# Performance work log

Measured on AMD Instinct MI355X. Metric: run time of the kernel, lower is better.

## Reference

```python
import jax, jax.numpy as jnp
import numpy as np

N_EMBD = 512
N_EXPERTS = 4
TOP_K = 2
D_FF = 4 * N_EMBD


def setup_inputs() -> dict:
    key = jax.random.key(0)
    k_x, k_g, k_w1, k_w2 = jax.random.split(key, 4)
    b, t = 8, 2048
    x = jax.random.normal(k_x, (b, t, N_EMBD), dtype=jnp.float32)
    # Linear layers are bias-free; kaiming-uniform-ish init scale
    gate_w = jax.random.normal(k_g, (N_EMBD, N_EXPERTS), dtype=jnp.float32) * (1.0 / np.sqrt(N_EMBD))
    w1 = jax.random.normal(k_w1, (N_EXPERTS, N_EMBD, D_FF), dtype=jnp.float32) * (1.0 / np.sqrt(N_EMBD))
    w2 = jax.random.normal(k_w2, (N_EXPERTS, D_FF, N_EMBD), dtype=jnp.float32) * (1.0 / np.sqrt(D_FF))
    return {"x": x, "gate_w": gate_w, "w1": w1, "w2": w2}


def reference(x, gate_w, w1, w2):
    # Eval mode: UnitCenteredNoise and Dropout are identity.
    b, t, c = x.shape
    xf = x.reshape(b * t, c)                         # [N, C]
    n = xf.shape[0]

    gate_logits = xf @ gate_w                        # [N, E]
    gate_probs = jax.nn.softmax(gate_logits, axis=-1)
    top_w, top_i = jax.lax.top_k(gate_probs, TOP_K)  # [N, K]
    top_w = top_w / jnp.clip(jnp.sum(top_w, axis=-1, keepdims=True), 1e-6)

    # Sparse router weights [N, E]: zeros except normalized top-k probs.
    router_sparse = jnp.zeros((n, N_EXPERTS), dtype=top_w.dtype)
    router_sparse = router_sparse.at[jnp.arange(n)[:, None], top_i].set(top_w)

    # Per-expert MLP on all tokens, combined with the sparse router weights.
    # Mathematically identical to the masked dispatch/combine in the original.
    h = jnp.einsum('nc,ech->enh', xf, w1)            # [E, N, 4C]
    h = jax.nn.gelu(h, approximate=False)            # torch F.gelu default = erf
    y = jnp.einsum('enh,ehc->enc', h, w2)            # [E, N, C]
    out_flat = jnp.einsum('ne,enc->nc', router_sparse, y)

    return out_flat.reshape(b, t, c), router_sparse
```

## Files before the change

### kernel.cpp

```cpp
#include <hip/hip_runtime.h>
#include <hip/hip_fp16.h>


#define NTOK  16384
#define CDIM  512
#define FF    2048
#define NEXP  4
#define CAP   33280
#define NBLK  260
#define BM    128
#define BN1   128
#define BN2   128
#define BK    32
#define CPAD  32

typedef _Float16 f16;
typedef __attribute__((ext_vector_type(8))) _Float16 f16x8;
typedef __attribute__((ext_vector_type(4))) _Float16 f16x4;
typedef __attribute__((ext_vector_type(4))) float f32x4;

__device__ __forceinline__ void gload16(const void* g, void* l) {
  __builtin_amdgcn_global_load_lds(
      (const __attribute__((address_space(1))) unsigned int*)g,
      (__attribute__((address_space(3))) unsigned int*)l, 16, 0, 0);
}

__device__ __forceinline__ float gelu_fast(float v) {
  float az = fabsf(v) * 0.7071067811865476f;
  float t = __builtin_amdgcn_rcpf(fmaf(0.3275911f, az, 1.0f));
  float p = fmaf(fmaf(fmaf(fmaf(1.061405429f, t, -1.453152027f), t,
                           1.421413741f), t, -0.284496736f), t, 0.254829592f) * t;
  float e = __builtin_amdgcn_exp2f(az * az * -1.4426950408889634f);
  float erfa = fmaf(-p, e, 1.0f);
  float u = copysignf(erfa, v);
  return 0.5f * v * (1.0f + u);
}

__device__ __forceinline__ int xcd_swz(int bid, int nwg) {
  int q = nwg >> 3, r = nwg & 7;
  int x = bid & 7, o = bid >> 3;
  return (x < r ? x * (q + 1) : r * (q + 1) + (x - r) * q) + o;
}


__global__ __launch_bounds__(256) void k_init(int* list, int* cnt) {
  int i = blockIdx.x * 256 + threadIdx.x;
  if (i < CAP) list[i] = -1;
  if (i < 4) cnt[i * CPAD] = 0;
}

__global__ __launch_bounds__(256) void k_cast_t(const float* __restrict__ in,
                                                f16* __restrict__ out, int R, int Cc) {
  __shared__ f16 T[64][72];
  int ez = blockIdx.z;
  const float* ine = in + (size_t)ez * R * Cc;
  f16* oute = out + (size_t)ez * R * Cc;
  int c0 = blockIdx.x * 64;
  int r0 = blockIdx.y * 64;
  int t = threadIdx.x;
  {
    int rr = t >> 2, cc = (t & 3) * 16;
    const float* src = ine + (size_t)(r0 + rr) * Cc + c0 + cc;
    union { f16 h[16]; uint4 u[2]; } pk;
#pragma unroll
    for (int j = 0; j < 16; j += 4) {
      float4 a = *(const float4*)(src + j);
      pk.h[j] = (f16)a.x; pk.h[j + 1] = (f16)a.y;
      pk.h[j + 2] = (f16)a.z; pk.h[j + 3] = (f16)a.w;
    }
    *(uint4*)&T[rr][cc] = pk.u[0];
    *(uint4*)&T[rr][cc + 8] = pk.u[1];
  }
  __syncthreads();
  {
    int oc = t >> 2, orr = (t & 3) * 16;
    union { f16 h[16]; uint4 u[2]; } pk;
#pragma unroll
    for (int j = 0; j < 16; ++j) pk.h[j] = T[orr + j][oc];
    f16* dst = oute + (size_t)(c0 + oc) * R + r0 + orr;
    *(uint4*)dst = pk.u[0];
    *(uint4*)(dst + 8) = pk.u[1];
  }
}


__global__ __launch_bounds__(256) void k_router(const float* __restrict__ x,
                                                const float* __restrict__ gw,
                                                f16* __restrict__ xh,
                                                float* __restrict__ rout,
                                                float4* __restrict__ tokinfo,
                                                int* __restrict__ cnt) {
  __shared__ int lcnt[4];
  int tid = threadIdx.x;
  if (tid < 4) lcnt[tid] = 0;
  __syncthreads();
  int wv = tid >> 6, lane = tid & 63;
  const float4* g = ((const float4*)gw) + lane * 8;
  float4 gv[8];
#pragma unroll
  for (int j = 0; j < 8; ++j) gv[j] = g[j];

  int tok0 = blockIdx.x * 64 + wv * 16;
  for (int i = 0; i < 16; ++i) {
    int tok = tok0 + i;
    const float4* xr = (const float4*)(x + (size_t)tok * CDIM + lane * 8);
    float4 a0 = xr[0], a1 = xr[1];
    union { f16 h[8]; uint4 u; } pk;
    pk.h[0] = (f16)a0.x; pk.h[1] = (f16)a0.y; pk.h[2] = (f16)a0.z; pk.h[3] = (f16)a0.w;
    pk.h[4] = (f16)a1.x; pk.h[5] = (f16)a1.y; pk.h[6] = (f16)a1.z; pk.h[7] = (f16)a1.w;
    *(uint4*)(xh + (size_t)tok * CDIM + lane * 8) = pk.u;
    float xv[8] = {a0.x, a0.y, a0.z, a0.w, a1.x, a1.y, a1.z, a1.w};
    float l0 = 0, l1 = 0, l2 = 0, l3 = 0;
#pragma unroll
    for (int j = 0; j < 8; ++j) {
      float4 g4 = gv[j];
      l0 = fmaf(xv[j], g4.x, l0); l1 = fmaf(xv[j], g4.y, l1);
      l2 = fmaf(xv[j], g4.z, l2); l3 = fmaf(xv[j], g4.w, l3);
    }
#pragma unroll
    for (int off = 32; off; off >>= 1) {
      l0 += __shfl_xor(l0, off); l1 += __shfl_xor(l1, off);
      l2 += __shfl_xor(l2, off); l3 += __shfl_xor(l3, off);
    }
    if (lane == 0) {
      float lg[4] = {l0, l1, l2, l3};
      float m = fmaxf(fmaxf(lg[0], lg[1]), fmaxf(lg[2], lg[3]));
      float p[4], s = 0.f;
#pragma unroll
      for (int e = 0; e < 4; ++e) { p[e] = expf(lg[e] - m); s += p[e]; }
      int i0 = 0;
#pragma unroll
      for (int e = 1; e < 4; ++e) if (lg[e] > lg[i0]) i0 = e;
      int i1 = -1;
#pragma unroll
      for (int e = 0; e < 4; ++e)
        if (e != i0 && (i1 < 0 || lg[e] > lg[i1])) i1 = e;
      float p0 = p[i0] / s, p1 = p[i1] / s;
      float ss = fmaxf(p0 + p1, 1e-6f);
      float w0 = p0 / ss, w1v = p1 / ss;
      float r[4] = {0.f, 0.f, 0.f, 0.f};
      r[i0] = w0; r[i1] = w1v;
      *(float4*)(rout + tok * 4) = make_float4(r[0], r[1], r[2], r[3]);
      float4 ti;
      ti.x = __int_as_float(i0); ti.y = __int_as_float(i1); ti.z = w0; ti.w = w1v;
      tokinfo[tok] = ti;
      atomicAdd(&lcnt[i0], 1);
      atomicAdd(&lcnt[i1], 1);
    }
  }
  __syncthreads();
  if (tid < 4) atomicAdd(cnt + tid * CPAD, lcnt[tid]);
}

__global__ void k_bases(const int* __restrict__ cnt, int* __restrict__ base,
                        int* __restrict__ cursor) {
  if (threadIdx.x == 0 && blockIdx.x == 0) {
    int b = 0;
#pragma unroll
    for (int e = 0; e < 4; ++e) {
      base[e] = b; cursor[e * CPAD] = b;
      b += (cnt[e * CPAD] + 127) & ~127;
    }
    base[4] = b;
  }
}

__global__ __launch_bounds__(256) void k_assign(const float4* __restrict__ tokinfo,
                                                int* cursor, int* __restrict__ list,
                                                int2* __restrict__ tokslot) {
  __shared__ int lcnt[4], lbase[4];
  int tid = threadIdx.x;
  if (tid < 4) lcnt[tid] = 0;
  __syncthreads();
  int t0 = blockIdx.x * 1024 + tid * 4;
  float4 ti[4]; int lo0[4], lo1[4];
#pragma unroll
  for (int j = 0; j < 4; ++j) {
    ti[j] = tokinfo[t0 + j];
    lo0[j] = atomicAdd(&lcnt[__float_as_int(ti[j].x)], 1);
    lo1[j] = atomicAdd(&lcnt[__float_as_int(ti[j].y)], 1);
  }
  __syncthreads();
  if (tid < 4) lbase[tid] = atomicAdd(cursor + tid * CPAD, lcnt[tid]);
  __syncthreads();
#pragma unroll
  for (int j = 0; j < 4; ++j) {
    int s0 = lbase[__float_as_int(ti[j].x)] + lo0[j];
    list[s0] = t0 + j;
    int s1 = lbase[__float_as_int(ti[j].y)] + lo1[j];
    list[s1] = t0 + j;
    tokslot[t0 + j] = make_int2(s0, s1);
  }
}


__global__ __launch_bounds__(256, 4) void k_gemm1(const f16* __restrict__ xh,
                                                  const f16* __restrict__ w1t,
                                                  const int* __restrict__ list,
                                                  const int* __restrict__ base,
                                                  f16* __restrict__ H, int cb, int nwg) {
  __shared__ __align__(16) char smem[32768 + 512];
  int* slist = (int*)(smem + 32768);
  int tid = threadIdx.x;
  int wk = xcd_swz(blockIdx.x, nwg);
  int bx = wk >> 4, by = wk & 15;
  int m0 = (cb + bx) * BM;
  int mloc = bx * BM;
  int h0 = by * BN1;
  int e = 0;
#pragma unroll
  for (int i = 1; i < 4; ++i) if (m0 >= base[i]) e = i;
  if (tid < BM) {
    int v = list[m0 + tid];
    slist[tid] = v < 0 ? 0 : v;
  }
  __syncthreads();

  int tokr[2];
#pragma unroll
  for (int i = 0; i < 2; ++i) tokr[i] = slist[i * 64 + (tid >> 2)];

  const f16* wB = w1t + (size_t)(e * FF + h0) * CDIM;
  int kbs = ((tid & 3) * 16) ^ (((tid >> 3) & 3) << 4);

  f32x4 acc[4][4] = {};
  int lane = tid & 63, w = tid >> 6, wr = w >> 1, wc = w & 1;

  auto stage = [&](int kk, int p) {
    char* s = smem + p * 16384;
#pragma unroll
    for (int i = 0; i < 2; ++i) {
      gload16(xh + (size_t)tokr[i] * CDIM + kk * BK + (kbs >> 1),
              s + i * 4096 + tid * 16);
    }
#pragma unroll
    for (int i = 0; i < 2; ++i) {
      int row = i * 64 + (tid >> 2);
      gload16(wB + (size_t)row * CDIM + kk * BK + (kbs >> 1),
              s + 8192 + i * 4096 + tid * 16);
    }
  };

  auto compute = [&](int p) {
    const char* s = smem + p * 16384;
    f16x8 af[4], bfr[4];
    int kb = (lane >> 4) * 16;
#pragma unroll
    for (int fr = 0; fr < 4; ++fr) {
      int row = wr * 64 + fr * 16 + (lane & 15);
      af[fr] = *(const f16x8*)(s + row * 64 + (kb ^ (((row >> 1) & 3) << 4)));
    }
#pragma unroll
    for (int fc = 0; fc < 4; ++fc) {
      int col = wc * 64 + fc * 16 + (lane & 15);
      bfr[fc] = *(const f16x8*)(s + 8192 + col * 64 + (kb ^ (((col >> 1) & 3) << 4)));
    }
#pragma unroll
    for (int fr = 0; fr < 4; ++fr)
#pragma unroll
      for (int fc = 0; fc < 4; ++fc)
        acc[fr][fc] = __builtin_amdgcn_mfma_f32_16x16x32_f16(af[fr], bfr[fc],
                                                             acc[fr][fc], 0, 0, 0);
  };

  stage(0, 0);
  __syncthreads();
  for (int kk = 0; kk < 16; ++kk) {
    if (kk < 15) stage(kk + 1, (kk + 1) & 1);
    __builtin_amdgcn_sched_barrier(0);
    __builtin_amdgcn_s_setprio(1);
    compute(kk & 1);
    __builtin_amdgcn_s_setprio(0);
    __syncthreads();
  }

#pragma unroll
  for (int fr = 0; fr < 4; ++fr)
#pragma unroll
    for (int fc = 0; fc < 4; ++fc)
#pragma unroll
      for (int i = 0; i < 4; ++i) {
        int row = wr * 64 + fr * 16 + (lane >> 4) * 4 + i;
        int col = wc * 64 + fc * 16 + (lane & 15);
        float v = gelu_fast(acc[fr][fc][i]);
        int off = (row * 256 + col * 2) ^ ((row & 7) << 4);
        *(f16*)(smem + off) = (f16)v;
      }
  __syncthreads();
#pragma unroll
  for (int j = 0; j < 8; ++j) {
    int row = j * 16 + (tid >> 4);
    int colb = ((tid & 15) * 16) ^ ((row & 7) << 4);
    uint4 v = *(const uint4*)(smem + row * 256 + colb);
    *(uint4*)((char*)H + ((size_t)(mloc + row) * FF + h0) * 2 + (tid & 15) * 16) = v;
  }
}


__global__ __launch_bounds__(256, 4) void k_gemm2(const f16* __restrict__ H,
                                                  const f16* __restrict__ w2t,
                                                  const int* __restrict__ base,
                                                  f16* __restrict__ Y, int cb, int nwg) {
  __shared__ __align__(16) char smem[32768];
  int tid = threadIdx.x;
  int wk = xcd_swz(blockIdx.x, nwg);
  int bx = wk >> 2, by = wk & 3;
  int m0 = (cb + bx) * BM;
  int mloc = bx * BM;
  int c0 = by * BN2;
  int e = 0;
#pragma unroll
  for (int i = 1; i < 4; ++i) if (m0 >= base[i]) e = i;

  const f16* pA = H + (size_t)mloc * FF;
  const f16* wB = w2t + (size_t)(e * CDIM + c0) * FF;
  int kbs = ((tid & 3) * 16) ^ (((tid >> 3) & 3) << 4);

  f32x4 acc[4][4] = {};
  int lane = tid & 63, w = tid >> 6, wr = w >> 1, wc = w & 1;

  auto stage = [&](int kk, int p) {
    char* s = smem + p * 16384;
#pragma unroll
    for (int i = 0; i < 2; ++i) {
      int row = i * 64 + (tid >> 2);
      gload16(pA + (size_t)row * FF + kk * BK + (kbs >> 1),
              s + i * 4096 + tid * 16);
    }
#pragma unroll
    for (int i = 0; i < 2; ++i) {
      int row = i * 64 + (tid >> 2);
      gload16(wB + (size_t)row * FF + kk * BK + (kbs >> 1),
              s + 8192 + i * 4096 + tid * 16);
    }
  };

  auto compute = [&](int p) {
    const char* s = smem + p * 16384;
    f16x8 af[4], bfr[4];
    int kb = (lane >> 4) * 16;
#pragma unroll
    for (int fr = 0; fr < 4; ++fr) {
      int row = wr * 64 + fr * 16 + (lane & 15);
      af[fr] = *(const f16x8*)(s + row * 64 + (kb ^ (((row >> 1) & 3) << 4)));
    }
#pragma unroll
    for (int fc = 0; fc < 4; ++fc) {
      int col = wc * 64 + fc * 16 + (lane & 15);
      bfr[fc] = *(const f16x8*)(s + 8192 + col * 64 + (kb ^ (((col >> 1) & 3) << 4)));
    }
#pragma unroll
    for (int fr = 0; fr < 4; ++fr)
#pragma unroll
      for (int fc = 0; fc < 4; ++fc)
        acc[fr][fc] = __builtin_amdgcn_mfma_f32_16x16x32_f16(af[fr], bfr[fc],
                                                             acc[fr][fc], 0, 0, 0);
  };

  stage(0, 0);
  __syncthreads();
  for (int kk = 0; kk < 64; ++kk) {
    if (kk < 63) stage(kk + 1, (kk + 1) & 1);
    __builtin_amdgcn_sched_barrier(0);
    __builtin_amdgcn_s_setprio(1);
    compute(kk & 1);
    __builtin_amdgcn_s_setprio(0);
    __syncthreads();
  }

#pragma unroll
  for (int fr = 0; fr < 4; ++fr)
#pragma unroll
    for (int fc = 0; fc < 4; ++fc)
#pragma unroll
      for (int i = 0; i < 4; ++i) {
        int row = wr * 64 + fr * 16 + (lane >> 4) * 4 + i;
        int col = wc * 64 + fc * 16 + (lane & 15);
        int off = (row * 256 + col * 2) ^ ((row & 7) << 4);
        *(f16*)(smem + off) = (f16)acc[fr][fc][i];
      }
  __syncthreads();
#pragma unroll
  for (int j = 0; j < 8; ++j) {
    int row = j * 16 + (tid >> 4);
    int colb = ((tid & 15) * 16) ^ ((row & 7) << 4);
    uint4 v = *(const uint4*)(smem + row * 256 + colb);
    *(uint4*)((char*)Y + ((size_t)(m0 + row) * CDIM + c0) * 2 + (tid & 15) * 16) = v;
  }
}


__global__ __launch_bounds__(256) void k_combine(const f16* __restrict__ Y,
                                                 const float4* __restrict__ tokinfo,
                                                 const int2* __restrict__ tokslot,
                                                 float* __restrict__ out) {
  int gid = blockIdx.x * 256 + threadIdx.x;
  int tok = gid >> 7;
  int cc = (gid & 127) * 4;
  int2 sl = tokslot[tok];
  float4 ti = tokinfo[tok];
  f16x4 y0 = *(const f16x4*)(Y + (size_t)sl.x * CDIM + cc);
  f16x4 y1 = *(const f16x4*)(Y + (size_t)sl.y * CDIM + cc);
  float w0 = ti.z, w1 = ti.w;
  float4 o;
  o.x = w0 * (float)y0[0] + w1 * (float)y1[0];
  o.y = w0 * (float)y0[1] + w1 * (float)y1[1];
  o.z = w0 * (float)y0[2] + w1 * (float)y1[2];
  o.w = w0 * (float)y0[3] + w1 * (float)y1[3];
  *(float4*)(out + (size_t)tok * CDIM + cc) = o;
}


extern "C" void kernel_launch(void* const* d_in, const int* in_sizes, int n_in,
                              void* d_out, int out_size, void* d_ws, size_t ws_size,
                              hipStream_t stream) {
  const float* x  = (const float*)d_in[0];
  const float* gw = (const float*)d_in[1];
  const float* w1 = (const float*)d_in[2];
  const float* w2 = (const float*)d_in[3];
  float* out  = (float*)d_out;
  float* rout = out + (size_t)NTOK * CDIM;

  char* ws = (char*)d_ws;
  f16* xh      = (f16*)ws;      ws += (size_t)NTOK * CDIM * 2;
  f16* w1t     = (f16*)ws;      ws += (size_t)NEXP * FF * CDIM * 2;
  f16* w2t     = (f16*)ws;      ws += (size_t)NEXP * FF * CDIM * 2;
  f16* Ybuf    = (f16*)ws;      ws += (size_t)CAP * CDIM * 2;
  float4* tokinfo = (float4*)ws; ws += (size_t)NTOK * 16;
  int2* tokslot = (int2*)ws;    ws += (size_t)NTOK * 8;
  int* list    = (int*)ws;      ws += (size_t)CAP * 4;
  int* cnt     = (int*)ws;      ws += 4 * CPAD * 4;
  int* base    = (int*)ws;      ws += 64;
  int* cursor  = (int*)ws;      ws += 4 * CPAD * 4;
  f16* Hbuf    = (f16*)ws;

  size_t base_bytes = (size_t)(ws - (char*)d_ws);
  const int opts[12] = {260, 130, 65, 52, 26, 20, 13, 10, 5, 4, 2, 1};
  int CB = 1;
  for (int oi = 0; oi < 12; ++oi) {
    if (base_bytes + (size_t)opts[oi] * BM * FF * 2 <= ws_size) { CB = opts[oi]; break; }
  }

  k_init<<<(CAP + 255) / 256, 256, 0, stream>>>(list, cnt);
  k_cast_t<<<dim3(FF / 64, CDIM / 64, NEXP), 256, 0, stream>>>(w1, w1t, CDIM, FF);
  k_cast_t<<<dim3(CDIM / 64, FF / 64, NEXP), 256, 0, stream>>>(w2, w2t, FF, CDIM);
  k_router<<<NTOK / 64, 256, 0, stream>>>(x, gw, xh, rout, tokinfo, cnt);
  k_bases<<<1, 64, 0, stream>>>(cnt, base, cursor);
  k_assign<<<NTOK / 1024, 256, 0, stream>>>(tokinfo, cursor, list, tokslot);

  for (int cb = 0; cb < NBLK; cb += CB) {
    int n1 = CB * 16, n2 = CB * 4;
    k_gemm1<<<n1, 256, 0, stream>>>(xh, w1t, list, base, Hbuf, cb, n1);
    k_gemm2<<<n2, 256, 0, stream>>>(Hbuf, w2t, base, Ybuf, cb, n2);
  }
  k_combine<<<NTOK * CDIM / 4 / 256, 256, 0, stream>>>(Ybuf, tokinfo, tokslot, out);
}
```

Baseline: 264.5 us.

## Merge weight cast launches, drop init kernel, widen router grid and combine vectors

The two weight transpose-cast launches become one kernel whose z-dimension selects w1 or w2. The separate init kernel is removed: the router writes per-block expert counts to a buffer instead of using global atomics, and k_bases reduces them and fills only the padding slots of the list with -1. The router grid grows to 1024 blocks with 16 tokens each for more parallelism, and combine handles 8 halves per thread. The aim is fewer launches and better occupancy in small kernels. The risk is that unset list slots rely on k_assign filling every real slot.

Result: faster. 255.2 us (-3.5%).

```diff
diff --git a/kernel.cpp b/kernel.cpp
--- a/kernel.cpp
+++ b/kernel.cpp
@@ -13,6 +13,7 @@
 #define BN2   128
 #define BK    32
 #define CPAD  32
+#define RBLK  1024
 
 typedef _Float16 f16;
 typedef __attribute__((ext_vector_type(8))) _Float16 f16x8;
@@ -43,20 +44,19 @@
 }
 
 
-__global__ __launch_bounds__(256) void k_init(int* list, int* cnt) {
-  int i = blockIdx.x * 256 + threadIdx.x;
-  if (i < CAP) list[i] = -1;
-  if (i < 4) cnt[i * CPAD] = 0;
-}
-
-__global__ __launch_bounds__(256) void k_cast_t(const float* __restrict__ in,
-                                                f16* __restrict__ out, int R, int Cc) {
+__global__ __launch_bounds__(256) void k_cast_t2(const float* __restrict__ w1,
+                                                 f16* __restrict__ w1t,
+                                                 const float* __restrict__ w2,
+                                                 f16* __restrict__ w2t) {
   __shared__ f16 T[64][72];
-  int ez = blockIdx.z;
+  int z = blockIdx.z;
+  const float* in; f16* out; int R, Cc, ez, c0, r0;
+  if (z < 4) { in = w1; out = w1t; R = CDIM; Cc = FF; ez = z;
+               c0 = blockIdx.x * 64; r0 = blockIdx.y * 64; }
+  else       { in = w2; out = w2t; R = FF; Cc = CDIM; ez = z - 4;
+               c0 = blockIdx.y * 64; r0 = blockIdx.x * 64; }
   const float* ine = in + (size_t)ez * R * Cc;
   f16* oute = out + (size_t)ez * R * Cc;
-  int c0 = blockIdx.x * 64;
-  int r0 = blockIdx.y * 64;
   int t = threadIdx.x;
   {
     int rr = t >> 2, cc = (t & 3) * 16;
@@ -89,7 +89,7 @@
                                                 f16* __restrict__ xh,
                                                 float* __restrict__ rout,
                                                 float4* __restrict__ tokinfo,
-                                                int* __restrict__ cnt) {
+                                                int* __restrict__ bcnt) {
   __shared__ int lcnt[4];
   int tid = threadIdx.x;
   if (tid < 4) lcnt[tid] = 0;
@@ -100,8 +100,8 @@
 #pragma unroll
   for (int j = 0; j < 8; ++j) gv[j] = g[j];
 
-  int tok0 = blockIdx.x * 64 + wv * 16;
-  for (int i = 0; i < 16; ++i) {
+  int tok0 = blockIdx.x * 16 + wv * 4;
+  for (int i = 0; i < 4; ++i) {
     int tok = tok0 + i;
     const float4* xr = (const float4*)(x + (size_t)tok * CDIM + lane * 8);
     float4 a0 = xr[0], a1 = xr[1];
@@ -149,19 +149,39 @@
     }
   }
   __syncthreads();
-  if (tid < 4) atomicAdd(cnt + tid * CPAD, lcnt[tid]);
-}
-
-__global__ void k_bases(const int* __restrict__ cnt, int* __restrict__ base,
-                        int* __restrict__ cursor) {
-  if (threadIdx.x == 0 && blockIdx.x == 0) {
+  if (tid < 4) bcnt[blockIdx.x * 4 + tid] = lcnt[tid];
+}
+
+__global__ __launch_bounds__(256) void k_bases(const int* __restrict__ bcnt,
+                                               int* __restrict__ base,
+                                               int* __restrict__ cursor,
+                                               int* __restrict__ list) {
+  __shared__ int tot[4], lb[5];
+  int tid = threadIdx.x;
+  if (tid < 4) tot[tid] = 0;
+  __syncthreads();
+  int acc[4] = {0, 0, 0, 0};
+  for (int i = tid; i < RBLK; i += 256) {
+    const int4 v = *(const int4*)(bcnt + i * 4);
+    acc[0] += v.x; acc[1] += v.y; acc[2] += v.z; acc[3] += v.w;
+  }
+#pragma unroll
+  for (int e = 0; e < 4; ++e) atomicAdd(&tot[e], acc[e]);
+  __syncthreads();
+  if (tid == 0) {
     int b = 0;
 #pragma unroll
     for (int e = 0; e < 4; ++e) {
-      base[e] = b; cursor[e * CPAD] = b;
-      b += (cnt[e * CPAD] + 127) & ~127;
-    }
-    base[4] = b;
+      lb[e] = b; base[e] = b; cursor[e * CPAD] = b;
+      b += (tot[e] + 127) & ~127;
+    }
+    lb[4] = b; base[4] = b;
+  }
+  __syncthreads();
+#pragma unroll
+  for (int e = 0; e < 4; ++e) {
+    int s = lb[e] + tot[e], end = lb[e + 1];
+    for (int i = s + tid; i < end; i += 256) list[i] = -1;
   }
 }
 
@@ -395,19 +415,25 @@
                                                  const int2* __restrict__ tokslot,
                                                  float* __restrict__ out) {
   int gid = blockIdx.x * 256 + threadIdx.x;
-  int tok = gid >> 7;
-  int cc = (gid & 127) * 4;
+  int tok = gid >> 6;
+  int cc = (gid & 63) * 8;
   int2 sl = tokslot[tok];
   float4 ti = tokinfo[tok];
-  f16x4 y0 = *(const f16x4*)(Y + (size_t)sl.x * CDIM + cc);
-  f16x4 y1 = *(const f16x4*)(Y + (size_t)sl.y * CDIM + cc);
+  f16x8 y0 = *(const f16x8*)(Y + (size_t)sl.x * CDIM + cc);
+  f16x8 y1 = *(const f16x8*)(Y + (size_t)sl.y * CDIM + cc);
   float w0 = ti.z, w1 = ti.w;
-  float4 o;
-  o.x = w0 * (float)y0[0] + w1 * (float)y1[0];
-  o.y = w0 * (float)y0[1] + w1 * (float)y1[1];
-  o.z = w0 * (float)y0[2] + w1 * (float)y1[2];
-  o.w = w0 * (float)y0[3] + w1 * (float)y1[3];
-  *(float4*)(out + (size_t)tok * CDIM + cc) = o;
+  float4 o0, o1;
+  o0.x = w0 * (float)y0[0] + w1 * (float)y1[0];
+  o0.y = w0 * (float)y0[1] + w1 * (float)y1[1];
+  o0.z = w0 * (float)y0[2] + w1 * (float)y1[2];
+  o0.w = w0 * (float)y0[3] + w1 * (float)y1[3];
+  o1.x = w0 * (float)y0[4] + w1 * (float)y1[4];
+  o1.y = w0 * (float)y0[5] + w1 * (float)y1[5];
+  o1.z = w0 * (float)y0[6] + w1 * (float)y1[6];
+  o1.w = w0 * (float)y0[7] + w1 * (float)y1[7];
+  float* orow = out + (size_t)tok * CDIM + cc;
+  *(float4*)orow = o0;
+  *(float4*)(orow + 4) = o1;
 }
 
 
@@ -429,7 +455,7 @@
   float4* tokinfo = (float4*)ws; ws += (size_t)NTOK * 16;
   int2* tokslot = (int2*)ws;    ws += (size_t)NTOK * 8;
   int* list    = (int*)ws;      ws += (size_t)CAP * 4;
-  int* cnt     = (int*)ws;      ws += 4 * CPAD * 4;
+  int* bcnt    = (int*)ws;      ws += (size_t)RBLK * 4 * 4;
   int* base    = (int*)ws;      ws += 64;
   int* cursor  = (int*)ws;      ws += 4 * CPAD * 4;
   f16* Hbuf    = (f16*)ws;
@@ -441,11 +467,9 @@
     if (base_bytes + (size_t)opts[oi] * BM * FF * 2 <= ws_size) { CB = opts[oi]; break; }
   }
 
-  k_init<<<(CAP + 255) / 256, 256, 0, stream>>>(list, cnt);
-  k_cast_t<<<dim3(FF / 64, CDIM / 64, NEXP), 256, 0, stream>>>(w1, w1t, CDIM, FF);
-  k_cast_t<<<dim3(CDIM / 64, FF / 64, NEXP), 256, 0, stream>>>(w2, w2t, FF, CDIM);
-  k_router<<<NTOK / 64, 256, 0, stream>>>(x, gw, xh, rout, tokinfo, cnt);
-  k_bases<<<1, 64, 0, stream>>>(cnt, base, cursor);
+  k_cast_t2<<<dim3(FF / 64, CDIM / 64, 8), 256, 0, stream>>>(w1, w1t, w2, w2t);
+  k_router<<<RBLK, 256, 0, stream>>>(x, gw, xh, rout, tokinfo, bcnt);
+  k_bases<<<1, 256, 0, stream>>>(bcnt, base, cursor, list);
   k_assign<<<NTOK / 1024, 256, 0, stream>>>(tokinfo, cursor, list, tokslot);
 
   for (int cb = 0; cb < NBLK; cb += CB) {
@@ -453,5 +477,5 @@
     k_gemm1<<<n1, 256, 0, stream>>>(xh, w1t, list, base, Hbuf, cb, n1);
     k_gemm2<<<n2, 256, 0, stream>>>(Hbuf, w2t, base, Ybuf, cb, n2);
   }
-  k_combine<<<NTOK * CDIM / 4 / 256, 256, 0, stream>>>(Ybuf, tokinfo, tokslot, out);
-}
+  k_combine<<<NTOK * CDIM / 8 / 256, 256, 0, stream>>>(Ybuf, tokinfo, tokslot, out);
+}
```
